# Optimization experiments

Measured on AMD Instinct MI355X. Metric: run time of the kernel, lower is better.

Reference implementation:

```python
import jax, jax.numpy as jnp
import numpy as np

B, T, D, H, L, F = 128, 512, 32, 128, 3, 4


def setup_inputs() -> dict:
    key = jax.random.key(0)
    ks = jax.random.split(key, 13)
    s = 0.05
    inp = {
        "x": jax.random.normal(ks[0], (B, T, D), dtype=jnp.float32),
        # layer 0 input weights [4H, D]; layers 1..L-1 input weights [L-1, 4H, H]
        "w_ih0": jax.random.normal(ks[1], (4 * H, D), dtype=jnp.float32) * s,
        "w_ih_rest": jax.random.normal(ks[2], (L - 1, 4 * H, H), dtype=jnp.float32) * s,
        "w_hh": jax.random.normal(ks[3], (L, 4 * H, H), dtype=jnp.float32) * s,
        "b_ih": jax.random.normal(ks[4], (L, 4 * H), dtype=jnp.float32) * s,
        "b_hh": jax.random.normal(ks[5], (L, 4 * H), dtype=jnp.float32) * s,
        "w_attn": jax.random.normal(ks[6], (1, H), dtype=jnp.float32) * s,
        "b_attn": jax.random.normal(ks[7], (1,), dtype=jnp.float32) * s,
        "w1": jax.random.normal(ks[8], (64, H), dtype=jnp.float32) * s,
        "b1": jax.random.normal(ks[9], (64,), dtype=jnp.float32) * s,
        "w2": jax.random.normal(ks[10], (F, 64), dtype=jnp.float32) * s,
        "b2": jax.random.normal(ks[11], (F,), dtype=jnp.float32) * s,
    }
    return inp


def _lstm_layer(xs, w_ih, w_hh, bi, bh):
    # xs: [B, T, Din] -> hs: [B, T, H]; PyTorch gate order i, f, g, o
    b, t = xs.shape[0], xs.shape[1]
    h_dim = w_hh.shape[1]
    pre = jnp.einsum('bti,gi->btg', xs, w_ih) + bi + bh  # [B, T, 4H]

    def step(carry, p_t):
        h, c = carry
        g = p_t + h @ w_hh.T
        i, f, gg, o = jnp.split(g, 4, axis=-1)
        i = jax.nn.sigmoid(i)
        f = jax.nn.sigmoid(f)
        gg = jnp.tanh(gg)
        o = jax.nn.sigmoid(o)
        c = f * c + i * gg
        h = o * jnp.tanh(c)
        return (h, c), h

    h0 = jnp.zeros((b, h_dim), xs.dtype)
    _, hs = jax.lax.scan(step, (h0, h0), jnp.swapaxes(pre, 0, 1))
    return jnp.swapaxes(hs, 0, 1)


def reference(x, w_ih0, w_ih_rest, w_hh, b_ih, b_hh, w_attn, b_attn, w1, b1, w2, b2):
    out = _lstm_layer(x, w_ih0, w_hh[0], b_ih[0], b_hh[0])
    for l in range(1, L):
        out = _lstm_layer(out, w_ih_rest[l - 1], w_hh[l], b_ih[l], b_hh[l])
    # additive attention pooling over time
    attn_w = jax.nn.softmax(jnp.einsum('bth,oh->bto', out, w_attn) + b_attn, axis=1)  # [B,T,1]
    ctx = jnp.sum(attn_w * out, axis=1)  # [B, H]
    # MLP head (dropout is identity at inference)
    h1 = jax.nn.relu(ctx @ w1.T + b1)
    return h1 @ w2.T + b2
```

## Files before the change

kernel.cpp:

```cpp
#include <hip/hip_runtime.h>
#include <math.h>

#define Bn 128
#define Tn 512
#define Dn 32
#define Hn 128
#define Gn 512
#define Ln 3

#define BAR_LDS() asm volatile("s_waitcnt lgkmcnt(0)\n\ts_barrier" ::: "memory")

typedef _Float16 h2 __attribute__((ext_vector_type(2)));
typedef _Float16 half8 __attribute__((ext_vector_type(8)));
typedef float f32x4 __attribute__((ext_vector_type(4)));

__device__ __forceinline__ float dot2(h2 a, h2 b, float c) {
    return __builtin_amdgcn_fdot2(a, b, c, false);
}
__device__ __forceinline__ h2 pkh(float a, float b) {
    h2 r; r.x = (_Float16)a; r.y = (_Float16)b; return r;
}
__device__ __forceinline__ float sigm(float x) {
    return __builtin_amdgcn_rcpf(1.f + __expf(-x));
}
__device__ __forceinline__ float tanh_fast(float x) {
    return 1.f - 2.f * __builtin_amdgcn_rcpf(1.f + __expf(2.f * x));
}

#define DPPADD(a, CTRL) { \
    int _t = __builtin_amdgcn_update_dpp(0, __builtin_bit_cast(int, a), \
                                         CTRL, 0xF, 0xF, true); \
    a += __builtin_bit_cast(float, _t); }

#define KEEPH(x) asm volatile("" : "+v"(x))
#define DECL16(P, R) \
  h2 P##0=pkh(R[0],R[1]),   P##1=pkh(R[2],R[3]),   P##2=pkh(R[4],R[5]),   P##3=pkh(R[6],R[7]),   \
     P##4=pkh(R[8],R[9]),   P##5=pkh(R[10],R[11]), P##6=pkh(R[12],R[13]), P##7=pkh(R[14],R[15]), \
     P##8=pkh(R[16],R[17]), P##9=pkh(R[18],R[19]), P##10=pkh(R[20],R[21]),P##11=pkh(R[22],R[23]),\
     P##12=pkh(R[24],R[25]),P##13=pkh(R[26],R[27]),P##14=pkh(R[28],R[29]),P##15=pkh(R[30],R[31]);
#define KEEP16(P) \
  KEEPH(P##0); KEEPH(P##1); KEEPH(P##2); KEEPH(P##3); KEEPH(P##4); KEEPH(P##5); \
  KEEPH(P##6); KEEPH(P##7); KEEPH(P##8); KEEPH(P##9); KEEPH(P##10); KEEPH(P##11); \
  KEEPH(P##12); KEEPH(P##13); KEEPH(P##14); KEEPH(P##15);

#define DOT4V(j) { \
    aI = dot2(hv##j, wi##j, aI);                 \
    aF = dot2(hv##j, wf##j, aF);                 \
    aG = dot2(hv##j, wg##j, aG);                 \
    aO = dot2(hv##j, wo##j, aO); }

__global__ __launch_bounds__(256) void cvt_f2h(
    const float* __restrict__ in, _Float16* __restrict__ out, int n)
{
    int base = (blockIdx.x * 256 + threadIdx.x) * 4;
    if (base < n) {
        float4 v = *(const float4*)(in + base);
        *(h2*)(out + base)     = pkh(v.x, v.y);
        *(h2*)(out + base + 2) = pkh(v.z, v.w);
    }
}

__global__ __launch_bounds__(256) void gemm_pre_mfma(
    const _Float16* __restrict__ A, int K, int rowStrideB, int t0, int tlog,
    const _Float16* __restrict__ W,
    const float* __restrict__ bi, const float* __restrict__ bh,
    float* __restrict__ C)
{
    __shared__ h2 As2[64][20];
    __shared__ h2 Bs2[64][20];
    const int tid  = threadIdx.x;
    const int row0 = blockIdx.x * 64;
    const int col0 = blockIdx.y * 64;
    const int w    = tid >> 6;
    const int lane = tid & 63;
    const int qm   = (w >> 1) * 32;
    const int qn   = (w & 1) * 32;
    const int fm   = lane & 15;
    const int fq   = lane >> 4;
    const int tmask = (1 << tlog) - 1;
    const int lrow = tid >> 2;
    const int lk   = (tid & 3) * 8;

    f32x4 acc00 = {0,0,0,0}, acc01 = {0,0,0,0};
    f32x4 acc10 = {0,0,0,0}, acc11 = {0,0,0,0};

    for (int k0 = 0; k0 < K; k0 += 32) {
        {
            int rg = row0 + lrow;
            int b_idx = rg >> tlog, tt = rg & tmask;
            const _Float16* ap = A + (size_t)b_idx * rowStrideB +
                                 (size_t)(t0 + tt) * K + (k0 + lk);
            *(float4*)&As2[lrow][(tid & 3) * 4] = *(const float4*)ap;
            const _Float16* wp = W + (size_t)(col0 + lrow) * K + (k0 + lk);
            *(float4*)&Bs2[lrow][(tid & 3) * 4] = *(const float4*)wp;
        }
        __syncthreads();
        half8 a0 = *(const half8*)&As2[qm + fm][fq * 4];
        half8 a1 = *(const half8*)&As2[qm + 16 + fm][fq * 4];
        half8 b0 = *(const half8*)&Bs2[qn + fm][fq * 4];
        half8 b1 = *(const half8*)&Bs2[qn + 16 + fm][fq * 4];
        acc00 = __builtin_amdgcn_mfma_f32_16x16x32_f16(a0, b0, acc00, 0, 0, 0);
        acc01 = __builtin_amdgcn_mfma_f32_16x16x32_f16(a0, b1, acc01, 0, 0, 0);
        acc10 = __builtin_amdgcn_mfma_f32_16x16x32_f16(a1, b0, acc10, 0, 0, 0);
        acc11 = __builtin_amdgcn_mfma_f32_16x16x32_f16(a1, b1, acc11, 0, 0, 0);
        __syncthreads();
    }

    const int g0 = col0 + qn + fm;
    const int g1 = g0 + 16;
    const float bb0 = bi[g0] + bh[g0];
    const float bb1 = bi[g1] + bh[g1];
    const int m0 = row0 + qm + fq * 4;
    #pragma unroll
    for (int r = 0; r < 4; r++) {
        C[(size_t)(m0 + r) * Gn + g0]      = acc00[r] + bb0;
        C[(size_t)(m0 + r) * Gn + g1]      = acc01[r] + bb1;
        C[(size_t)(m0 + 16 + r) * Gn + g0] = acc10[r] + bb0;
        C[(size_t)(m0 + 16 + r) * Gn + g1] = acc11[r] + bb1;
    }
}

__global__ __launch_bounds__(512)
__attribute__((amdgpu_waves_per_eu(2, 2)))
void lstm_scan(
    const float* __restrict__ pre,
    const float* __restrict__ w_hh,
    _Float16* __restrict__ hs16,
    float* __restrict__ h_state, float* __restrict__ c_state,
    int t0, int TCH, int first)
{
    const int b    = blockIdx.x;
    const int tid  = threadIdx.x;
    const int lane = tid & 63;
    const int wv   = tid >> 6;
    const int kq   = lane & 3;
    const int u    = wv * 16 + (lane >> 2);

    __shared__ h2 hbuf[2][Hn / 2];

    const float* rI = w_hh + (size_t)(0 * Hn + u) * Hn + kq * 32;
    const float* rF = w_hh + (size_t)(1 * Hn + u) * Hn + kq * 32;
    const float* rG = w_hh + (size_t)(2 * Hn + u) * Hn + kq * 32;
    const float* rO = w_hh + (size_t)(3 * Hn + u) * Hn + kq * 32;
    DECL16(wi, rI) DECL16(wf, rF) DECL16(wg, rG) DECL16(wo, rO)
    KEEP16(wi) KEEP16(wf) KEEP16(wg) KEEP16(wo)

    float cr = first ? 0.f : c_state[b * Hn + u];
    if (tid < Hn / 2) {
        h2 hv = pkh(0.f, 0.f);
        if (!first) hv = pkh(h_state[b * Hn + 2 * tid],
                             h_state[b * Hn + 2 * tid + 1]);
        hbuf[0][tid] = hv;
    }
    __syncthreads();

    const float* pp = pre + (size_t)b * TCH * Gn + kq * Hn + u;
    _Float16* hswr = hs16 + ((size_t)b * Tn + t0) * Hn + u;

    const float mI = (kq == 0) ? 1.f : 0.f;
    const float mF = (kq == 1) ? 1.f : 0.f;
    const float mG = (kq == 2) ? 1.f : 0.f;
    const float mO = (kq == 3) ? 1.f : 0.f;

    float hlast = 0.f;

    auto body = [&](int t, float pv) {
        const h2* hrow = &hbuf[t & 1][kq * 16];
        half8 hAv = *(const half8*)(hrow);
        half8 hBv = *(const half8*)(hrow + 4);
        half8 hCv = *(const half8*)(hrow + 8);
        half8 hDv = *(const half8*)(hrow + 12);
        h2 hv0  = ((const h2*)&hAv)[0], hv1  = ((const h2*)&hAv)[1];
        h2 hv2  = ((const h2*)&hAv)[2], hv3  = ((const h2*)&hAv)[3];
        h2 hv4  = ((const h2*)&hBv)[0], hv5  = ((const h2*)&hBv)[1];
        h2 hv6  = ((const h2*)&hBv)[2], hv7  = ((const h2*)&hBv)[3];
        h2 hv8  = ((const h2*)&hCv)[0], hv9  = ((const h2*)&hCv)[1];
        h2 hv10 = ((const h2*)&hCv)[2], hv11 = ((const h2*)&hCv)[3];
        h2 hv12 = ((const h2*)&hDv)[0], hv13 = ((const h2*)&hDv)[1];
        h2 hv14 = ((const h2*)&hDv)[2], hv15 = ((const h2*)&hDv)[3];

        float aI = 0.f, aF = 0.f, aG = 0.f, aO = 0.f;
        DOT4V(0)  DOT4V(1)  DOT4V(2)  DOT4V(3)
        DOT4V(4)  DOT4V(5)  DOT4V(6)  DOT4V(7)
        DOT4V(8)  DOT4V(9)  DOT4V(10) DOT4V(11)
        DOT4V(12) DOT4V(13) DOT4V(14) DOT4V(15)

        aI = fmaf(pv, mI, aI);
        aF = fmaf(pv, mF, aF);
        aG = fmaf(pv, mG, aG);
        aO = fmaf(pv, mO, aO);

        DPPADD(aI, 0xB1) DPPADD(aF, 0xB1) DPPADD(aG, 0xB1) DPPADD(aO, 0xB1)
        DPPADD(aI, 0x4E) DPPADD(aF, 0x4E) DPPADD(aG, 0x4E) DPPADD(aO, 0x4E)

        float iv = sigm(aI);
        float fv = sigm(aF);
        float gv = tanh_fast(aG);
        float ov = sigm(aO);
        cr = fv * cr + iv * gv;
        float hnew = ov * tanh_fast(cr);
        hlast = hnew;
        _Float16 hh = (_Float16)hnew;
        if (kq == 0) {
            ((_Float16*)hbuf[(t + 1) & 1])[u] = hh;
            *hswr = hh;
        }
        hswr += Hn;
        BAR_LDS();
    };

    float p0 = pp[0];
    float p1 = (TCH > 1) ? pp[Gn] : p0;
    const float* pld = pp + 2 * (size_t)Gn;

    const int TCH2 = TCH - 2;
    for (int t = 0; t < TCH2; t++) {
        float pv = p0; p0 = p1;
        p1 = *pld; pld += Gn;
        body(t, pv);
    }
    { float pv = p0; p0 = p1; body(TCH2, pv); }
    body(TCH2 + 1, p0);

    if (kq == 0) {
        h_state[b * Hn + u] = hlast;
        c_state[b * Hn + u] = cr;
    }
}

__global__ __launch_bounds__(256) void head_kernel(
    const _Float16* __restrict__ hs16,
    const float* __restrict__ w_attn, const float* __restrict__ b_attn,
    const float* __restrict__ w1, const float* __restrict__ b1,
    const float* __restrict__ w2, const float* __restrict__ b2,
    float* __restrict__ out)
{
    const int b = blockIdx.x;
    const int tid = threadIdx.x;
    __shared__ h2 wa2[Hn / 2];
    __shared__ __align__(16) float sc[Tn];
    __shared__ __align__(16) float red[256];
    __shared__ __align__(16) float ctx_sh[Hn];
    __shared__ __align__(16) float h1_sh[64];

    if (tid < Hn / 2) wa2[tid] = pkh(w_attn[2 * tid], w_attn[2 * tid + 1]);
    __syncthreads();

    const _Float16* hb = hs16 + (size_t)b * Tn * Hn;

    for (int t = tid; t < Tn; t += 256) {
        const h2* hp = (const h2*)(hb + (size_t)t * Hn);
        float s = 0.f;
        #pragma unroll
        for (int k = 0; k < 64; k++) s = dot2(hp[k], wa2[k], s);
        sc[t] = s + b_attn[0];
    }
    __syncthreads();

    float m = fmaxf(sc[tid], sc[tid + 256]);
    red[tid] = m; __syncthreads();
    for (int s_ = 128; s_ > 0; s_ >>= 1) {
        if (tid < s_) red[tid] = fmaxf(red[tid], red[tid + s_]);
        __syncthreads();
    }
    float mx = red[0];
    __syncthreads();
    float e0 = __expf(sc[tid] - mx), e1 = __expf(sc[tid + 256] - mx);
    sc[tid] = e0; sc[tid + 256] = e1;
    red[tid] = e0 + e1; __syncthreads();
    for (int s_ = 128; s_ > 0; s_ >>= 1) {
        if (tid < s_) red[tid] += red[tid + s_];
        __syncthreads();
    }
    float inv = 1.f / red[0];
    __syncthreads();

    {
        int jj = tid & 127, half = tid >> 7;
        float a = 0.f;
        for (int t = half * 256; t < half * 256 + 256; t++)
            a += sc[t] * (float)hb[(size_t)t * Hn + jj];
        red[tid] = a;
        __syncthreads();
        if (tid < Hn) ctx_sh[tid] = (red[tid] + red[tid + Hn]) * inv;
        __syncthreads();
    }

    if (tid < 64) {
        const float4* wvv = (const float4*)(w1 + (size_t)tid * Hn);
        const float4* cv = (const float4*)ctx_sh;
        float s = 0.f;
        #pragma unroll
        for (int k = 0; k < 32; k++) {
            float4 a = wvv[k], c = cv[k];
            s += a.x * c.x + a.y * c.y + a.z * c.z + a.w * c.w;
        }
        h1_sh[tid] = fmaxf(s + b1[tid], 0.f);
    }
    __syncthreads();

    if (tid < 4) {
        float s = 0.f;
        const float* wvv = w2 + tid * 64;
        #pragma unroll
        for (int k = 0; k < 64; k++) s += wvv[k] * h1_sh[k];
        out[b * 4 + tid] = s + b2[tid];
    }
}

extern "C" void kernel_launch(void* const* d_in, const int* in_sizes, int n_in,
                              void* d_out, int out_size, void* d_ws, size_t ws_size,
                              hipStream_t stream)
{
    const float* x        = (const float*)d_in[0];
    const float* w_ih0    = (const float*)d_in[1];
    const float* w_ih_rest= (const float*)d_in[2];
    const float* w_hh     = (const float*)d_in[3];
    const float* b_ih     = (const float*)d_in[4];
    const float* b_hh     = (const float*)d_in[5];
    const float* w_attn   = (const float*)d_in[6];
    const float* b_attn   = (const float*)d_in[7];
    const float* w1       = (const float*)d_in[8];
    const float* b1       = (const float*)d_in[9];
    const float* w2       = (const float*)d_in[10];
    const float* b2       = (const float*)d_in[11];
    float* out = (float*)d_out;

    const size_t nX  = (size_t)Bn * Tn * Dn;
    const size_t nHS = (size_t)Bn * Tn * Hn;
    const size_t nW0 = (size_t)Gn * Dn;
    const size_t nWR = (size_t)(Ln - 1) * Gn * Hn;

    float* ws   = (float*)d_ws;
    float* h_st = ws;
    float* c_st = h_st + (size_t)Bn * Hn;
    float* pre  = c_st + (size_t)Bn * Hn;

    const size_t halfBytes = (nX + nHS + nW0 + nWR) * sizeof(_Float16);
    int tch = 512;
    while (tch > 16) {
        size_t need = (2 * (size_t)Bn * Hn +
                       (size_t)Bn * tch * Gn) * sizeof(float) + halfBytes;
        if (need <= ws_size) break;
        tch >>= 1;
    }
    int tlog = 31 - __builtin_clz((unsigned)tch);

    _Float16* xh   = (_Float16*)(pre + (size_t)Bn * tch * Gn);
    _Float16* hs16 = xh + nX;
    _Float16* w0h  = hs16 + nHS;
    _Float16* wrh  = w0h + nW0;

    cvt_f2h<<<(int)((nX / 4 + 255) / 256), 256, 0, stream>>>(x, xh, (int)nX);
    cvt_f2h<<<(int)((nW0 / 4 + 255) / 256), 256, 0, stream>>>(w_ih0, w0h, (int)nW0);
    cvt_f2h<<<(int)((nWR / 4 + 255) / 256), 256, 0, stream>>>(w_ih_rest, wrh, (int)nWR);

    for (int l = 0; l < Ln; l++) {
        const _Float16* A = (l == 0) ? xh : hs16;
        int K = (l == 0) ? Dn : Hn;
        const _Float16* W = (l == 0) ? w0h : (wrh + (size_t)(l - 1) * Gn * Hn);
        const float* whl = w_hh + (size_t)l * Gn * Hn;
        for (int c = 0; c < Tn / tch; c++) {
            dim3 gg(Bn * tch / 64, 8);
            gemm_pre_mfma<<<gg, 256, 0, stream>>>(A, K, Tn * K, c * tch, tlog,
                                                  W, b_ih + l * Gn, b_hh + l * Gn, pre);
            lstm_scan<<<Bn, 512, 0, stream>>>(pre, whl, hs16, h_st, c_st,
                                              c * tch, tch, c == 0 ? 1 : 0);
        }
    }
    head_kernel<<<Bn, 256, 0, stream>>>(hs16, w_attn, b_attn, w1, b1, w2, b2, out);
}
```

Before: 1.071 ms.

## Fuse layers 0 and 1 into a wavefront-pipelined scan with flag sync

Adds a scan01 kernel that runs layer 0 and layer 1 concurrently as two block rows. Each computes its input projection in registers with fp16 dot2, and layer 1 spin-waits on per-batch atomic flags published by layer 0 every 8 steps. This drops the separate input GEMMs and serial launches for the first two layers and overlaps their recurrences. Layer 2 keeps the GEMM plus scan path but stores the preactivations in fp16. The costs are extra register pressure, global spin-waiting that assumes layer-0 and layer-1 blocks are co-resident, and lower precision for the preactivations.

```diff
diff --git a/kernel.cpp b/kernel.cpp
--- a/kernel.cpp
+++ b/kernel.cpp
@@ -33,6 +33,9 @@
     a += __builtin_bit_cast(float, _t); }
 
 #define KEEPH(x) asm volatile("" : "+v"(x))
+#define LD8H(p) (*(const half8*)(p))
+#define H2OF(V, i) (((const h2*)&(V))[i])
+
 #define DECL16(P, R) \
   h2 P##0=pkh(R[0],R[1]),   P##1=pkh(R[2],R[3]),   P##2=pkh(R[4],R[5]),   P##3=pkh(R[6],R[7]),   \
      P##4=pkh(R[8],R[9]),   P##5=pkh(R[10],R[11]), P##6=pkh(R[12],R[13]), P##7=pkh(R[14],R[15]), \
@@ -43,11 +46,40 @@
   KEEPH(P##6); KEEPH(P##7); KEEPH(P##8); KEEPH(P##9); KEEPH(P##10); KEEPH(P##11); \
   KEEPH(P##12); KEEPH(P##13); KEEPH(P##14); KEEPH(P##15);
 
+#define DECLIH(P, ROWF, ROW0) \
+  h2 P##0, P##1, P##2, P##3, P##4, P##5, P##6, P##7, \
+     P##8, P##9, P##10, P##11, P##12, P##13, P##14, P##15; \
+  if (layer) { \
+    const h2* _r = (const h2*)(ROWF); \
+    half8 _a = LD8H(_r), _b = LD8H(_r + 4), _c = LD8H(_r + 8), _d = LD8H(_r + 12); \
+    P##0 = H2OF(_a,0); P##1 = H2OF(_a,1); P##2  = H2OF(_a,2); P##3  = H2OF(_a,3); \
+    P##4 = H2OF(_b,0); P##5 = H2OF(_b,1); P##6  = H2OF(_b,2); P##7  = H2OF(_b,3); \
+    P##8 = H2OF(_c,0); P##9 = H2OF(_c,1); P##10 = H2OF(_c,2); P##11 = H2OF(_c,3); \
+    P##12= H2OF(_d,0); P##13= H2OF(_d,1); P##14 = H2OF(_d,2); P##15 = H2OF(_d,3); \
+  } else { \
+    half8 _a = LD8H((const h2*)(ROW0)); \
+    h2 _z = pkh(0.f, 0.f); \
+    P##0 = H2OF(_a,0); P##1 = H2OF(_a,1); P##2 = H2OF(_a,2); P##3 = H2OF(_a,3); \
+    P##4=_z; P##5=_z; P##6=_z; P##7=_z; P##8=_z; P##9=_z; P##10=_z; P##11=_z; \
+    P##12=_z; P##13=_z; P##14=_z; P##15=_z; \
+  }
+
+#define EXTRACT16(P, A, B, C, D) \
+  h2 P##0 = H2OF(A,0), P##1 = H2OF(A,1), P##2  = H2OF(A,2), P##3  = H2OF(A,3), \
+     P##4 = H2OF(B,0), P##5 = H2OF(B,1), P##6  = H2OF(B,2), P##7  = H2OF(B,3), \
+     P##8 = H2OF(C,0), P##9 = H2OF(C,1), P##10 = H2OF(C,2), P##11 = H2OF(C,3), \
+     P##12= H2OF(D,0), P##13= H2OF(D,1), P##14 = H2OF(D,2), P##15 = H2OF(D,3);
+
 #define DOT4V(j) { \
     aI = dot2(hv##j, wi##j, aI);                 \
     aF = dot2(hv##j, wf##j, aF);                 \
     aG = dot2(hv##j, wg##j, aG);                 \
     aO = dot2(hv##j, wo##j, aO); }
+#define DOT4Y(j) { \
+    aI = dot2(pv##j, yi##j, aI);                 \
+    aF = dot2(pv##j, yf##j, aF);                 \
+    aG = dot2(pv##j, yg##j, aG);                 \
+    aO = dot2(pv##j, yo##j, aO); }
 
 __global__ __launch_bounds__(256) void cvt_f2h(
     const float* __restrict__ in, _Float16* __restrict__ out, int n)
@@ -64,7 +96,7 @@
     const _Float16* __restrict__ A, int K, int rowStrideB, int t0, int tlog,
     const _Float16* __restrict__ W,
     const float* __restrict__ bi, const float* __restrict__ bh,
-    float* __restrict__ C)
+    _Float16* __restrict__ C)
 {
     __shared__ h2 As2[64][20];
     __shared__ h2 Bs2[64][20];
@@ -113,17 +145,172 @@
     const int m0 = row0 + qm + fq * 4;
     #pragma unroll
     for (int r = 0; r < 4; r++) {
-        C[(size_t)(m0 + r) * Gn + g0]      = acc00[r] + bb0;
-        C[(size_t)(m0 + r) * Gn + g1]      = acc01[r] + bb1;
-        C[(size_t)(m0 + 16 + r) * Gn + g0] = acc10[r] + bb0;
-        C[(size_t)(m0 + 16 + r) * Gn + g1] = acc11[r] + bb1;
+        C[(size_t)(m0 + r) * Gn + g0]      = (_Float16)(acc00[r] + bb0);
+        C[(size_t)(m0 + r) * Gn + g1]      = (_Float16)(acc01[r] + bb1);
+        C[(size_t)(m0 + 16 + r) * Gn + g0] = (_Float16)(acc10[r] + bb0);
+        C[(size_t)(m0 + 16 + r) * Gn + g1] = (_Float16)(acc11[r] + bb1);
+    }
+}
+
+__global__ __launch_bounds__(512)
+__attribute__((amdgpu_waves_per_eu(2)))
+void scan01(
+    const _Float16* __restrict__ xh,
+    const _Float16* __restrict__ w0h,
+    const _Float16* __restrict__ wrh,
+    const float* __restrict__ w_hh,
+    const float* __restrict__ b_ih, const float* __restrict__ b_hh,
+    _Float16* __restrict__ hs0,
+    _Float16* __restrict__ hs1,
+    int* __restrict__ flags)
+{
+    const int b     = blockIdx.x;
+    const int layer = blockIdx.y;
+    const int tid   = threadIdx.x;
+    const int lane  = tid & 63;
+    const int wv    = tid >> 6;
+    const int kq    = lane & 3;
+    const int u     = wv * 16 + (lane >> 2);
+
+    __shared__ h2 hbuf[2][Hn / 2];
+
+    const float* whl = w_hh + (size_t)layer * Gn * Hn;
+    const float* rI = whl + (size_t)(0 * Hn + u) * Hn + kq * 32;
+    const float* rF = whl + (size_t)(1 * Hn + u) * Hn + kq * 32;
+    const float* rG = whl + (size_t)(2 * Hn + u) * Hn + kq * 32;
+    const float* rO = whl + (size_t)(3 * Hn + u) * Hn + kq * 32;
+    DECL16(wi, rI) DECL16(wf, rF) DECL16(wg, rG) DECL16(wo, rO)
+    KEEP16(wi) KEEP16(wf) KEEP16(wg) KEEP16(wo)
+
+    DECLIH(yi, wrh + (size_t)(0 * Hn + u) * Hn + kq * 32,
+               w0h + (size_t)(0 * Hn + u) * Dn + kq * 8)
+    DECLIH(yf, wrh + (size_t)(1 * Hn + u) * Hn + kq * 32,
+               w0h + (size_t)(1 * Hn + u) * Dn + kq * 8)
+    DECLIH(yg, wrh + (size_t)(2 * Hn + u) * Hn + kq * 32,
+               w0h + (size_t)(2 * Hn + u) * Dn + kq * 8)
+    DECLIH(yo, wrh + (size_t)(3 * Hn + u) * Hn + kq * 32,
+               w0h + (size_t)(3 * Hn + u) * Dn + kq * 8)
+    KEEP16(yi) KEEP16(yf) KEEP16(yg) KEEP16(yo)
+
+    const float bI = b_ih[layer * Gn + 0 * Hn + u] + b_hh[layer * Gn + 0 * Hn + u];
+    const float bF = b_ih[layer * Gn + 1 * Hn + u] + b_hh[layer * Gn + 1 * Hn + u];
+    const float bG = b_ih[layer * Gn + 2 * Hn + u] + b_hh[layer * Gn + 2 * Hn + u];
+    const float bO = b_ih[layer * Gn + 3 * Hn + u] + b_hh[layer * Gn + 3 * Hn + u];
+
+    if (tid < Hn / 2) hbuf[0][tid] = pkh(0.f, 0.f);
+    __syncthreads();
+
+    _Float16* hswr = (layer ? hs1 : hs0) + (size_t)b * Tn * Hn + u;
+    const _Float16* hsin = hs0 + (size_t)b * Tn * Hn;
+    const _Float16* xrow = xh + (size_t)b * Tn * Dn;
+
+    float cr = 0.f;
+    int avail = 0;
+
+    auto gate = [&](int need) {
+        if (avail >= need) return;
+        do {
+            int a0 = 0;
+            if (lane == 0)
+                a0 = __hip_atomic_load(flags + b, __ATOMIC_ACQUIRE,
+                                       __HIP_MEMORY_SCOPE_AGENT);
+            avail = __builtin_amdgcn_readfirstlane(a0);
+            if (avail < need) __builtin_amdgcn_s_sleep(16);
+        } while (avail < need);
+    };
+
+    auto tick = [&](int t, half8 Pa, half8 Pb, half8 Pc, half8 Pd) {
+        const h2* hrow = &hbuf[t & 1][kq * 16];
+        half8 hA = LD8H(hrow);
+        half8 hB = LD8H(hrow + 4);
+        half8 hC = LD8H(hrow + 8);
+        half8 hD = LD8H(hrow + 12);
+        EXTRACT16(hv, hA, hB, hC, hD)
+        EXTRACT16(pv, Pa, Pb, Pc, Pd)
+
+        float aI = 0.f, aF = 0.f, aG = 0.f, aO = 0.f;
+        DOT4V(0)  DOT4V(1)  DOT4V(2)  DOT4V(3)
+        DOT4V(4)  DOT4V(5)  DOT4V(6)  DOT4V(7)
+        DOT4V(8)  DOT4V(9)  DOT4V(10) DOT4V(11)
+        DOT4V(12) DOT4V(13) DOT4V(14) DOT4V(15)
+        DOT4Y(0)  DOT4Y(1)  DOT4Y(2)  DOT4Y(3)
+        if (layer) {
+            DOT4Y(4)  DOT4Y(5)  DOT4Y(6)  DOT4Y(7)
+            DOT4Y(8)  DOT4Y(9)  DOT4Y(10) DOT4Y(11)
+            DOT4Y(12) DOT4Y(13) DOT4Y(14) DOT4Y(15)
+        }
+
+        DPPADD(aI, 0xB1) DPPADD(aF, 0xB1) DPPADD(aG, 0xB1) DPPADD(aO, 0xB1)
+        DPPADD(aI, 0x4E) DPPADD(aF, 0x4E) DPPADD(aG, 0x4E) DPPADD(aO, 0x4E)
+
+        float iv = sigm(aI + bI);
+        float fv = sigm(aF + bF);
+        float gv = tanh_fast(aG + bG);
+        float ov = sigm(aO + bO);
+        cr = fv * cr + iv * gv;
+        float hnew = ov * tanh_fast(cr);
+        _Float16 hh = (_Float16)hnew;
+        if (kq == 0) {
+            ((_Float16*)hbuf[(t + 1) & 1])[u] = hh;
+            *hswr = hh;
+        }
+        hswr += Hn;
+        BAR_LDS();
+    };
+
+    half8 pAa, pAb, pAc, pAd, pBa, pBb, pBc, pBd;
+    {
+        half8 z = {};
+        pAb = pAc = pAd = z;
+        pBb = pBc = pBd = z;
+    }
+    if (layer) {
+        gate(2);
+        const h2* r0 = (const h2*)(hsin + 0 * Hn + kq * 32);
+        pAa = LD8H(r0); pAb = LD8H(r0 + 4); pAc = LD8H(r0 + 8); pAd = LD8H(r0 + 12);
+        const h2* r1 = (const h2*)(hsin + 1 * Hn + kq * 32);
+        pBa = LD8H(r1); pBb = LD8H(r1 + 4); pBc = LD8H(r1 + 8); pBd = LD8H(r1 + 12);
+    } else {
+        pAa = LD8H((const h2*)(xrow + 0 * Dn + kq * 8));
+        pBa = LD8H((const h2*)(xrow + 1 * Dn + kq * 8));
+    }
+
+    for (int t = 0; t < Tn; t += 2) {
+        tick(t, pAa, pAb, pAc, pAd);
+
+        int r2 = (t + 2 < Tn) ? t + 2 : Tn - 1;
+        int r3 = (t + 3 < Tn) ? t + 3 : Tn - 1;
+        if (layer) {
+            int need = (t + 4 < Tn) ? t + 4 : Tn;
+            gate(need);
+            const h2* r = (const h2*)(hsin + (size_t)r2 * Hn + kq * 32);
+            pAa = LD8H(r); pAb = LD8H(r + 4); pAc = LD8H(r + 8); pAd = LD8H(r + 12);
+        } else {
+            pAa = LD8H((const h2*)(xrow + (size_t)r2 * Dn + kq * 8));
+        }
+
+        tick(t + 1, pBa, pBb, pBc, pBd);
+
+        if (layer) {
+            const h2* r = (const h2*)(hsin + (size_t)r3 * Hn + kq * 32);
+            pBa = LD8H(r); pBb = LD8H(r + 4); pBc = LD8H(r + 8); pBd = LD8H(r + 12);
+        } else {
+            pBa = LD8H((const h2*)(xrow + (size_t)r3 * Dn + kq * 8));
+            if (((t + 2) & 7) == 0) {
+                asm volatile("s_waitcnt vmcnt(0)" ::: "memory");
+                __syncthreads();
+                if (tid == 0)
+                    __hip_atomic_store(flags + b, t + 2, __ATOMIC_RELEASE,
+                                       __HIP_MEMORY_SCOPE_AGENT);
+            }
+        }
     }
 }
 
 __global__ __launch_bounds__(512)
 __attribute__((amdgpu_waves_per_eu(2, 2)))
 void lstm_scan(
-    const float* __restrict__ pre,
+    const _Float16* __restrict__ pre,
     const float* __restrict__ w_hh,
     _Float16* __restrict__ hs16,
     float* __restrict__ h_state, float* __restrict__ c_state,
@@ -154,7 +341,7 @@
     }
     __syncthreads();
 
-    const float* pp = pre + (size_t)b * TCH * Gn + kq * Hn + u;
+    const _Float16* pp = pre + (size_t)b * TCH * Gn + kq * Hn + u;
     _Float16* hswr = hs16 + ((size_t)b * Tn + t0) * Hn + u;
 
     const float mI = (kq == 0) ? 1.f : 0.f;
@@ -166,18 +353,11 @@
 
     auto body = [&](int t, float pv) {
         const h2* hrow = &hbuf[t & 1][kq * 16];
-        half8 hAv = *(const half8*)(hrow);
-        half8 hBv = *(const half8*)(hrow + 4);
-        half8 hCv = *(const half8*)(hrow + 8);
-        half8 hDv = *(const half8*)(hrow + 12);
-        h2 hv0  = ((const h2*)&hAv)[0], hv1  = ((const h2*)&hAv)[1];
-        h2 hv2  = ((const h2*)&hAv)[2], hv3  = ((const h2*)&hAv)[3];
-        h2 hv4  = ((const h2*)&hBv)[0], hv5  = ((const h2*)&hBv)[1];
-        h2 hv6  = ((const h2*)&hBv)[2], hv7  = ((const h2*)&hBv)[3];
-        h2 hv8  = ((const h2*)&hCv)[0], hv9  = ((const h2*)&hCv)[1];
-        h2 hv10 = ((const h2*)&hCv)[2], hv11 = ((const h2*)&hCv)[3];
-        h2 hv12 = ((const h2*)&hDv)[0], hv13 = ((const h2*)&hDv)[1];
-        h2 hv14 = ((const h2*)&hDv)[2], hv15 = ((const h2*)&hDv)[3];
+        half8 hAv = LD8H(hrow);
+        half8 hBv = LD8H(hrow + 4);
+        half8 hCv = LD8H(hrow + 8);
+        half8 hDv = LD8H(hrow + 12);
+        EXTRACT16(hv, hAv, hBv, hCv, hDv)
 
         float aI = 0.f, aF = 0.f, aG = 0.f, aO = 0.f;
         DOT4V(0)  DOT4V(1)  DOT4V(2)  DOT4V(3)
@@ -209,14 +389,14 @@
         BAR_LDS();
     };
 
-    float p0 = pp[0];
-    float p1 = (TCH > 1) ? pp[Gn] : p0;
-    const float* pld = pp + 2 * (size_t)Gn;
+    float p0 = (float)pp[0];
+    float p1 = (TCH > 1) ? (float)pp[Gn] : p0;
+    const _Float16* pld = pp + 2 * (size_t)Gn;
 
     const int TCH2 = TCH - 2;
     for (int t = 0; t < TCH2; t++) {
         float pv = p0; p0 = p1;
-        p1 = *pld; pld += Gn;
+        p1 = (float)*pld; pld += Gn;
         body(t, pv);
     }
     { float pv = p0; p0 = p1; body(TCH2, pv); }
@@ -330,43 +510,34 @@
     const size_t nHS = (size_t)Bn * Tn * Hn;
     const size_t nW0 = (size_t)Gn * Dn;
     const size_t nWR = (size_t)(Ln - 1) * Gn * Hn;
-
-    float* ws   = (float*)d_ws;
-    float* h_st = ws;
-    float* c_st = h_st + (size_t)Bn * Hn;
-    float* pre  = c_st + (size_t)Bn * Hn;
-
-    const size_t halfBytes = (nX + nHS + nW0 + nWR) * sizeof(_Float16);
-    int tch = 512;
-    while (tch > 16) {
-        size_t need = (2 * (size_t)Bn * Hn +
-                       (size_t)Bn * tch * Gn) * sizeof(float) + halfBytes;
-        if (need <= ws_size) break;
-        tch >>= 1;
-    }
-    int tlog = 31 - __builtin_clz((unsigned)tch);
-
-    _Float16* xh   = (_Float16*)(pre + (size_t)Bn * tch * Gn);
-    _Float16* hs16 = xh + nX;
-    _Float16* w0h  = hs16 + nHS;
+    const size_t nPRE = (size_t)Bn * Tn * Gn;
+
+    float* ws    = (float*)d_ws;
+    float* h_st  = ws;
+    float* c_st  = h_st + (size_t)Bn * Hn;
+    int*   flags = (int*)(c_st + (size_t)Bn * Hn);
+    _Float16* preh = (_Float16*)((float*)flags + 256);
+    _Float16* xh   = preh + nPRE;
+    _Float16* hs0  = xh + nX;
+    _Float16* hs1  = hs0 + nHS;
+    _Float16* hs2  = hs1 + nHS;
+    _Float16* w0h  = hs2 + nHS;
     _Float16* wrh  = w0h + nW0;
+
+    hipMemsetAsync(flags, 0, Bn * sizeof(int), stream);
 
     cvt_f2h<<<(int)((nX / 4 + 255) / 256), 256, 0, stream>>>(x, xh, (int)nX);
     cvt_f2h<<<(int)((nW0 / 4 + 255) / 256), 256, 0, stream>>>(w_ih0, w0h, (int)nW0);
     cvt_f2h<<<(int)((nWR / 4 + 255) / 256), 256, 0, stream>>>(w_ih_rest, wrh, (int)nWR);
 
-    for (int l = 0; l < Ln; l++) {
-        const _Float16* A = (l == 0) ? xh : hs16;
-        int K = (l == 0) ? Dn : Hn;
-        const _Float16* W = (l == 0) ? w0h : (wrh + (size_t)(l - 1) * Gn * Hn);
-        const float* whl = w_hh + (size_t)l * Gn * Hn;
-        for (int c = 0; c < Tn / tch; c++) {
-            dim3 gg(Bn * tch / 64, 8);
-            gemm_pre_mfma<<<gg, 256, 0, stream>>>(A, K, Tn * K, c * tch, tlog,
-                                                  W, b_ih + l * Gn, b_hh + l * Gn, pre);
-            lstm_scan<<<Bn, 512, 0, stream>>>(pre, whl, hs16, h_st, c_st,
-                                              c * tch, tch, c == 0 ? 1 : 0);
-        }
-    }
-    head_kernel<<<Bn, 256, 0, stream>>>(hs16, w_attn, b_attn, w1, b1, w2, b2, out);
-}
+    scan01<<<dim3(Bn, 2), 512, 0, stream>>>(xh, w0h, wrh, w_hh, b_ih, b_hh,
+                                            hs0, hs1, flags);
+
+    gemm_pre_mfma<<<dim3(Bn * Tn / 64, 8), 256, 0, stream>>>(
+        hs1, Hn, Tn * Hn, 0, 9,
+        wrh + (size_t)Gn * Hn, b_ih + 2 * Gn, b_hh + 2 * Gn, preh);
+    lstm_scan<<<Bn, 512, 0, stream>>>(preh, w_hh + 2 * (size_t)Gn * Hn,
+                                      hs2, h_st, c_st, 0, Tn, 1);
+
+    head_kernel<<<Bn, 256, 0, stream>>>(hs2, w_attn, b_attn, w1, b1, w2, b2, out);
+}
```

Result: no change. 1.088 ms (+1.5%).
